# Kernel optimization log

Measured on AMD Instinct MI355X. Metric: run time of the kernel, lower is better.

The kernel has to match this reference:

```python
import jax, jax.numpy as jnp
import numpy as np
from jax import lax


def setup_inputs() -> dict:
    key = jax.random.key(0)
    k1, k2 = jax.random.split(key)
    B, C_out, C_in, K, H, W = 16, 128, 128, 3, 64, 64
    features = jax.random.normal(k1, (B, C_in, H, W), dtype=jnp.float32)
    dynamic_kernel = jax.random.normal(k2, (B, C_out, C_in, K, K), dtype=jnp.float32)
    return {"features": features, "dynamic_kernel": dynamic_kernel}


def reference(features, dynamic_kernel):
    # Per-sample dynamic conv. unfold+bmm in torch == cross-correlation (conv2d)
    # with the per-sample kernel; we express it as a vmapped implicit-GEMM conv
    # instead of materializing the (C_in*K*K, H*W) unfold buffer.
    padding = 1

    def conv_one(x, w):  # x: (C_in, H, W), w: (C_out, C_in, K, K)
        return lax.conv_general_dilated(
            x[None],                      # (1, C_in, H, W)
            w,
            window_strides=(1, 1),
            padding=[(padding, padding), (padding, padding)],
            dimension_numbers=("NCHW", "OIHW", "NCHW"),
        )[0]                              # (C_out, H, W)

    return jax.vmap(conv_one)(features, dynamic_kernel)  # (B, C_out, H, W)
```

## Files before the change

### kernel.cpp

```cpp
#include <hip/hip_runtime.h>
#include <stdint.h>

#define BATCH 16
#define CIN   128
#define COUT  128
#define IMG_H 64
#define IMG_W 64
#define HW    4096
#define KTOT  1152
#define XH    66
#define XW    66
#define NCQ   16
#define NSTEPS 18
#define ASTEP 8192

typedef __attribute__((ext_vector_type(8))) __bf16 bf16x8;
typedef __attribute__((ext_vector_type(4))) float  f32x4;
typedef __attribute__((address_space(1))) const void* gas_p;
typedef __attribute__((address_space(3))) void*       las_p;

static __device__ __forceinline__ unsigned short f2bf(float f) {
  union { float f; uint32_t u; } c; c.f = f;
  uint32_t r = c.u + 0x7fffu + ((c.u >> 16) & 1u);
  return (unsigned short)(r >> 16);
}

static __device__ __forceinline__ void gload_lds16(const unsigned short* g, unsigned short* l) {
  __builtin_amdgcn_global_load_lds((gas_p)g, (las_p)l, 16, 0, 0);
}

__global__ void prep_fused(const float* __restrict__ x, const float* __restrict__ w,
                           unsigned short* __restrict__ wt4, unsigned short* __restrict__ xpad) {
  const int t = threadIdx.x;
  if (blockIdx.x < BATCH * IMG_H) {
    __shared__ uint32_t tile[64 * 68];
    const int b = blockIdx.x >> 6;
    const int h = blockIdx.x & 63;
    const float* xb = x + (size_t)b * CIN * HW + h * IMG_W;
    uint4* xp4 = (uint4*)xpad;

    const int lane16 = t & 15;
    const int g      = t >> 4;
#pragma unroll
    for (int it = 0; it < 4; ++it) {
      const int ci = it * 32 + g * 2;
      const float4 va = *(const float4*)(xb + (size_t)ci * HW + lane16 * 4);
      const float4 vb = *(const float4*)(xb + (size_t)(ci + 1) * HW + lane16 * 4);
      const float av[4] = {va.x, va.y, va.z, va.w};
      const float bv[4] = {vb.x, vb.y, vb.z, vb.w};
#pragma unroll
      for (int cc = 0; cc < 4; ++cc)
        tile[(lane16 * 4 + cc) * 68 + it * 16 + g] =
            (uint32_t)f2bf(av[cc]) | ((uint32_t)f2bf(bv[cc]) << 16);
    }
    __syncthreads();

    const uint32_t rbase = ((uint32_t)b * XH + h + 1) * NCQ;
#pragma unroll
    for (int it = 0; it < 4; ++it) {
      const int o   = it * 256 + t;
      const int cqg = o >> 6;
      const int wc  = o & 63;
      const uint4 v = *(const uint4*)&tile[wc * 68 + cqg * 4];
      xp4[(rbase + cqg) * XW + wc + 1] = v;
    }
    if (t < 32) {
      const int cqg = t & 15;
      const int col = (t >> 4) ? 65 : 0;
      xp4[(rbase + cqg) * XW + col] = make_uint4(0, 0, 0, 0);
    }
    if (h == 0) {
      const uint32_t r0  = (uint32_t)b * XH * NCQ * XW;
      const uint32_t r65 = ((uint32_t)b * XH + 65) * NCQ * XW;
      for (int i = t; i < NCQ * XW; i += 256) {
        xp4[r0 + i]  = make_uint4(0, 0, 0, 0);
        xp4[r65 + i] = make_uint4(0, 0, 0, 0);
      }
    }
  } else {
    const int idx  = blockIdx.x - BATCH * IMG_H;
    const int b    = idx / NSTEPS;
    const int step = idx % NSTEPS;
    const int khkw = step >> 1;
    const int cib  = (step & 1) << 6;
    const float* wb = w + (size_t)b * COUT * KTOT;
    unsigned short* dst = wt4 + ((size_t)b * NSTEPS + step) * ASTEP;
#pragma unroll
    for (int i = 0; i < 4; ++i) {
      const int c  = i * 256 + t;
      const int cq = c >> 7;
      const int co = c & 127;
      const int ci0 = cib + cq * 8;
      const float* src = wb + (size_t)co * KTOT + (size_t)ci0 * 9 + khkw;
      uint32_t p[4];
#pragma unroll
      for (int e = 0; e < 4; ++e)
        p[e] = (uint32_t)f2bf(src[(2 * e) * 9]) | ((uint32_t)f2bf(src[(2 * e + 1) * 9]) << 16);
      *(uint4*)&dst[(size_t)c * 8] = make_uint4(p[0], p[1], p[2], p[3]);
    }
  }
}

__global__ __launch_bounds__(512, 4) void dynconv_gemm(
    const unsigned short* __restrict__ wt4,
    const unsigned short* __restrict__ xpad,
    float* __restrict__ out) {
  __shared__ alignas(16) unsigned short SH[4][ASTEP];

  const int t   = threadIdx.x;
  const int bid = blockIdx.x;
  const int xcd = bid & 7;
  const int idx = bid >> 3;
  const int b   = xcd * 2 + (idx >> 5);
  const int oh0 = (idx & 31) * 2;

  const int lane = t & 63;
  const int wave = t >> 6;
  const int wm   = (wave & 1) << 6;
  const int wn   = ((wave >> 1) & 1) << 6;
  const int kg   = wave >> 2;
  const int l15  = lane & 15;
  const int quad = lane >> 4;

  const unsigned short* wt4b = wt4 + (size_t)b * NSTEPS * ASTEP;
  const unsigned short* xb   = xpad + (size_t)b * XH * NCQ * XW * 8;

#define STAGE(U, S)                                                           \
  {                                                                           \
    const int khkw_ = (S) >> 1;                                               \
    const int kh_   = (khkw_ * 11) >> 5;                                      \
    const int kw_   = khkw_ - kh_ * 3;                                        \
    const int cqb_  = ((S) & 1) << 3;                                         \
    const unsigned short* astep_ = wt4b + (size_t)(S) * ASTEP;                \
    _Pragma("unroll")                                                         \
    for (int r_ = 0; r_ < 2; ++r_) {                                          \
      gload_lds16(astep_ + (size_t)(r_ * 512 + t) * 8,                        \
                  &SH[U][(r_ * 512 + wave * 64) * 8]);                        \
      const unsigned short* bs_ = xb +                                        \
          ((size_t)((oh0 + (wave & 1) + kh_) * NCQ + cqb_ + r_ * 4 +          \
                    (wave >> 1)) * XW + kw_ + lane) * 8;                      \
      gload_lds16(bs_, &SH[2 + (U)][(r_ * 512 + wave * 64) * 8]);             \
    }                                                                         \
  }

  f32x4 acc[4][4] = {};

  STAGE(0, 0);
  __syncthreads();

#pragma unroll 2
  for (int s = 0; s < NSTEPS; ++s) {
    const int u = s & 1;
    if (s + 1 < NSTEPS) STAGE(u ^ 1, s + 1);

    const int cq = kg * 4 + quad;
    const unsigned short* a_ = &SH[u][0];
    const unsigned short* b_ = &SH[2 + u][0];
    bf16x8 af[4], bf[4];
#pragma unroll
    for (int i = 0; i < 4; ++i)
      af[i] = *(const bf16x8*)&a_[(cq * 128 + wm + i * 16 + l15) * 8];
#pragma unroll
    for (int j = 0; j < 4; ++j)
      bf[j] = *(const bf16x8*)&b_[(cq * 128 + wn + j * 16 + l15) * 8];
#pragma unroll
    for (int i = 0; i < 4; ++i)
#pragma unroll
      for (int j = 0; j < 4; ++j)
        acc[i][j] = __builtin_amdgcn_mfma_f32_16x16x32_bf16(af[i], bf[j], acc[i][j], 0, 0, 0);

    __syncthreads();
  }
#undef STAGE

  float* red = (float*)&SH[0][0];
  if (wave >= 4) {
    float* row = red + (size_t)((wave - 4) * 64 + lane) * 64;
#pragma unroll
    for (int m = 0; m < 16; ++m)
      *(f32x4*)&row[((m + lane) & 15) * 4] = acc[m >> 2][m & 3];
  }
  __syncthreads();
  if (wave < 4) {
    const float* row = red + (size_t)(wave * 64 + lane) * 64;
#pragma unroll
    for (int m = 0; m < 16; ++m) {
      const f32x4 v = *(const f32x4*)&row[((m + lane) & 15) * 4];
      acc[m >> 2][m & 3] += v;
    }

    float* obase = out + (size_t)b * COUT * HW + (size_t)(oh0 + (wn >> 6)) * IMG_W;
#pragma unroll
    for (int i = 0; i < 4; ++i) {
#pragma unroll
      for (int r = 0; r < 4; ++r) {
        const int co = wm + i * 16 + quad * 4 + r;
        float* orow = obase + (size_t)co * HW;
#pragma unroll
        for (int j = 0; j < 4; ++j)
          orow[j * 16 + l15] = acc[i][j][r];
      }
    }
  }
}

__global__ void dynconv_naive(const float* __restrict__ x, const float* __restrict__ w,
                              float* __restrict__ out) {
  const int o   = blockIdx.x * 256 + threadIdx.x;
  const int pix = o & (HW - 1);
  const int co  = (o >> 12) & (COUT - 1);
  const int b   = o >> 19;
  const int oh  = pix >> 6, ow = pix & 63;
  const float* xb = x + (size_t)b * CIN * HW;
  const float* wb = w + ((size_t)b * COUT + co) * CIN * 9;
  float s = 0.f;
  for (int ci = 0; ci < CIN; ++ci) {
    const float* xc = xb + ci * HW;
    const float* wc = wb + ci * 9;
#pragma unroll
    for (int kh = 0; kh < 3; ++kh) {
      const int ih = oh + kh - 1;
      if ((unsigned)ih >= IMG_H) continue;
#pragma unroll
      for (int kw = 0; kw < 3; ++kw) {
        const int iw = ow + kw - 1;
        if ((unsigned)iw >= IMG_W) continue;
        s += xc[ih * IMG_W + iw] * wc[kh * 3 + kw];
      }
    }
  }
  out[o] = s;
}

extern "C" void kernel_launch(void* const* d_in, const int* in_sizes, int n_in,
                              void* d_out, int out_size, void* d_ws, size_t ws_size,
                              hipStream_t stream) {
  const float* x = (const float*)d_in[0];
  const float* w = (const float*)d_in[1];
  float* out = (float*)d_out;

  const size_t wt_bytes = (size_t)BATCH * NSTEPS * ASTEP * sizeof(unsigned short);
  const size_t xp_bytes = (size_t)BATCH * XH * NCQ * XW * 8 * sizeof(unsigned short);

  if (ws_size >= wt_bytes + xp_bytes) {
    unsigned short* wt4  = (unsigned short*)d_ws;
    unsigned short* xpad = (unsigned short*)((char*)d_ws + wt_bytes);
    prep_fused<<<BATCH * IMG_H + BATCH * NSTEPS, 256, 0, stream>>>(x, w, wt4, xpad);
    dynconv_gemm<<<512, 512, 0, stream>>>(wt4, xpad, out);
  } else {
    dynconv_naive<<<(BATCH * COUT * HW) / 256, 256, 0, stream>>>(x, w, out);
  }
}
```

Before: 119.6 us.

## Stage padded input rows once per kh and reuse across kw shifts

Instead of reloading a shifted input tile for every one of the 18 K-steps, the kernel now loads the full padded 66-wide input rows for each kh into shared memory once. The three kw shifts then read from that tile at a column offset. The weight tile stays double-buffered per step. This cuts global-to-LDS traffic for the activation operand, but the B-tile load for the next kh is no longer overlapped with compute and adds an extra barrier stall, while LDS usage grows.

Result: no change. 120.4 us (+0.7%).

```diff
diff --git a/kernel.cpp b/kernel.cpp
--- a/kernel.cpp
+++ b/kernel.cpp
@@ -13,6 +13,8 @@
 #define NCQ   16
 #define NSTEPS 18
 #define ASTEP 8192
+#define AOFF(u) ((u) * ASTEP)
+#define BOFF  16384
 
 typedef __attribute__((ext_vector_type(8))) __bf16 bf16x8;
 typedef __attribute__((ext_vector_type(4))) float  f32x4;
@@ -105,7 +107,7 @@
     const unsigned short* __restrict__ wt4,
     const unsigned short* __restrict__ xpad,
     float* __restrict__ out) {
-  __shared__ alignas(16) unsigned short SH[4][ASTEP];
+  __shared__ alignas(16) unsigned short SH[33280];
 
   const int t   = threadIdx.x;
   const int bid = blockIdx.x;
@@ -121,59 +123,83 @@
   const int kg   = wave >> 2;
   const int l15  = lane & 15;
   const int quad = lane >> 4;
+  const int rsel = (wave >> 1) & 1;
 
   const unsigned short* wt4b = wt4 + (size_t)b * NSTEPS * ASTEP;
   const unsigned short* xb   = xpad + (size_t)b * XH * NCQ * XW * 8;
 
-#define STAGE(U, S)                                                           \
+#define STAGE_A(U, G)                                                         \
   {                                                                           \
-    const int khkw_ = (S) >> 1;                                               \
-    const int kh_   = (khkw_ * 11) >> 5;                                      \
-    const int kw_   = khkw_ - kh_ * 3;                                        \
-    const int cqb_  = ((S) & 1) << 3;                                         \
-    const unsigned short* astep_ = wt4b + (size_t)(S) * ASTEP;                \
+    const unsigned short* astep_ = wt4b + (size_t)(G) * ASTEP;                \
     _Pragma("unroll")                                                         \
-    for (int r_ = 0; r_ < 2; ++r_) {                                          \
+    for (int r_ = 0; r_ < 2; ++r_)                                            \
       gload_lds16(astep_ + (size_t)(r_ * 512 + t) * 8,                        \
-                  &SH[U][(r_ * 512 + wave * 64) * 8]);                        \
-      const unsigned short* bs_ = xb +                                        \
-          ((size_t)((oh0 + (wave & 1) + kh_) * NCQ + cqb_ + r_ * 4 +          \
-                    (wave >> 1)) * XW + kw_ + lane) * 8;                      \
-      gload_lds16(bs_, &SH[2 + (U)][(r_ * 512 + wave * 64) * 8]);             \
+                  &SH[AOFF(U) + (r_ * 512 + wave * 64) * 8]);                 \
+  }
+
+#define STAGE_B(KH)                                                           \
+  {                                                                           \
+    _Pragma("unroll")                                                         \
+    for (int k_ = 0; k_ < 4; ++k_) {                                          \
+      const int p_   = wave * 4 + k_;                                         \
+      const int row_ = p_ >> 4;                                               \
+      const int cq_  = p_ & 15;                                               \
+      const unsigned short* src_ = xb +                                       \
+          ((size_t)((oh0 + row_ + (KH)) * NCQ + cq_) * XW + lane) * 8;        \
+      gload_lds16(src_, &SH[BOFF + p_ * (XW * 8)]);                           \
     }                                                                         \
+    if (t < 64) {                                                             \
+      const int seg_ = t >> 1;                                                \
+      const int c64_ = 64 + (t & 1);                                          \
+      const int row_ = seg_ >> 4;                                             \
+      const int cq_  = seg_ & 15;                                             \
+      const uint4 v_ = *(const uint4*)(xb +                                   \
+          ((size_t)((oh0 + row_ + (KH)) * NCQ + cq_) * XW + c64_) * 8);       \
+      *(uint4*)&SH[BOFF + (seg_ * XW + c64_) * 8] = v_;                       \
+    }                                                                         \
   }
 
   f32x4 acc[4][4] = {};
 
-  STAGE(0, 0);
+  STAGE_B(0);
+  STAGE_A(0, 0);
   __syncthreads();
 
+  for (int kh = 0; kh < 3; ++kh) {
 #pragma unroll 2
-  for (int s = 0; s < NSTEPS; ++s) {
-    const int u = s & 1;
-    if (s + 1 < NSTEPS) STAGE(u ^ 1, s + 1);
-
-    const int cq = kg * 4 + quad;
-    const unsigned short* a_ = &SH[u][0];
-    const unsigned short* b_ = &SH[2 + u][0];
-    bf16x8 af[4], bf[4];
-#pragma unroll
-    for (int i = 0; i < 4; ++i)
-      af[i] = *(const bf16x8*)&a_[(cq * 128 + wm + i * 16 + l15) * 8];
-#pragma unroll
-    for (int j = 0; j < 4; ++j)
-      bf[j] = *(const bf16x8*)&b_[(cq * 128 + wn + j * 16 + l15) * 8];
-#pragma unroll
-    for (int i = 0; i < 4; ++i)
+    for (int ss = 0; ss < 6; ++ss) {
+      const int g  = kh * 6 + ss;
+      const int u  = ss & 1;
+      const int kw = ss >> 1;
+      const int cqh = ss & 1;
+      if (g < NSTEPS - 1) STAGE_A(u ^ 1, g + 1);
+
+      const int cql = kg * 4 + quad;
+      bf16x8 af[4], bf[4];
+#pragma unroll
+      for (int i = 0; i < 4; ++i)
+        af[i] = *(const bf16x8*)&SH[AOFF(u) + (cql * 128 + wm + i * 16 + l15) * 8];
 #pragma unroll
       for (int j = 0; j < 4; ++j)
-        acc[i][j] = __builtin_amdgcn_mfma_f32_16x16x32_bf16(af[i], bf[j], acc[i][j], 0, 0, 0);
-
-    __syncthreads();
-  }
-#undef STAGE
-
-  float* red = (float*)&SH[0][0];
+        bf[j] = *(const bf16x8*)&SH[BOFF +
+            ((rsel * 16 + cqh * 8 + cql) * XW + kw + j * 16 + l15) * 8];
+#pragma unroll
+      for (int i = 0; i < 4; ++i)
+#pragma unroll
+        for (int j = 0; j < 4; ++j)
+          acc[i][j] = __builtin_amdgcn_mfma_f32_16x16x32_bf16(af[i], bf[j], acc[i][j], 0, 0, 0);
+
+      __syncthreads();
+    }
+    if (kh < 2) {
+      STAGE_B(kh + 1);
+      __syncthreads();
+    }
+  }
+#undef STAGE_A
+#undef STAGE_B
+
+  float* red = (float*)&SH[0];
   if (wave >= 4) {
     float* row = red + (size_t)((wave - 4) * 64 + lane) * 64;
 #pragma unroll
```
